# Performance work log

Measured on AMD Instinct MI355X. Metric: run time of the kernel, lower is better.

## Reference

```python
import jax, jax.numpy as jnp
import numpy as np
import math

H = 12  # num_heads
LOGIT_SCALE_MAX = math.log(1.0 / 0.01)  # ~4.60517


def setup_inputs() -> dict:
    key = jax.random.key(0)
    ks = jax.random.split(key, 4)
    L, N, C = 1024, 8, 768
    scale = (C // H) ** -0.5
    return {
        "x": jax.random.normal(ks[0], (L, N, C), jnp.float32),
        "in_proj_weight": jax.random.normal(ks[1], (3 * C, C), jnp.float32) * scale,
        "in_proj_bias": jnp.zeros((3 * C,), jnp.float32),
        "logit_scale": jnp.full((H, 1, 1), jnp.log(10.0), jnp.float32),
        "head_scale": jnp.ones((H, 1, 1), jnp.float32),
        "out_w": jax.random.normal(ks[2], (C, C), jnp.float32) * scale,
        "out_b": jnp.zeros((C,), jnp.float32),
    }


def _normalize(t, eps=1e-12):
    # torch F.normalize: x / max(||x||, eps)
    n = jnp.linalg.norm(t, axis=-1, keepdims=True)
    return t / jnp.maximum(n, eps)


def reference(x, in_proj_weight, in_proj_bias, logit_scale, head_scale, out_w, out_b):
    L, N, C = x.shape
    D = C // H
    qkv = x @ in_proj_weight.T + in_proj_bias  # (L, N, 3C)
    q, k, v = jnp.split(qkv, 3, axis=-1)

    def to_heads(t):  # (L, N, C) -> (N, H, L, D); matches view(L, N*H, D).transpose(0,1)
        return t.reshape(L, N, H, D).transpose(1, 2, 0, 3)

    q, k, v = to_heads(q), to_heads(k), to_heads(v)
    # scaled-cosine attention: cosine sim * clamped-exp learnable logit scale
    attn = jnp.einsum('nhld,nhmd->nhlm', _normalize(q), _normalize(k))  # (N,H,L,L)
    ls = jnp.exp(jnp.minimum(logit_scale, LOGIT_SCALE_MAX))  # (H,1,1)
    attn = attn * ls[None]
    attn = jax.nn.softmax(attn, axis=-1)
    o = jnp.einsum('nhlm,nhmd->nhld', attn, v)  # (N,H,L,D)
    o = o * head_scale[None]  # per-head scale
    o = o.transpose(2, 0, 1, 3).reshape(L, N, C)  # back to (L, N, C)
    return o @ out_w.T + out_b
```

## Files before the change

kernel.cpp:

```cpp
#include <hip/hip_runtime.h>
#include <stdint.h>
#include <math.h>

typedef unsigned short u16;
typedef _Float16 f16;
typedef __attribute__((ext_vector_type(4))) float f32x4;
typedef __attribute__((ext_vector_type(8))) f16 h8;
typedef __attribute__((ext_vector_type(4))) f16 h4;
typedef __attribute__((ext_vector_type(2))) f16 h2;
typedef __attribute__((ext_vector_type(2))) __fp16 fp16x2;
typedef __attribute__((ext_vector_type(4))) unsigned int u32x4;
typedef __attribute__((ext_vector_type(4))) unsigned short u16x4;
typedef __attribute__((ext_vector_type(8))) unsigned short u16x8;

typedef const __attribute__((address_space(1))) u16 gas_u16;
typedef __attribute__((address_space(3))) u16 las_u16;

#define MFMA32(a,b,c) __builtin_amdgcn_mfma_f32_16x16x32_f16((a),(b),(c),0,0,0)
#define MFMA16(a,b,c) __builtin_amdgcn_mfma_f32_16x16x16f16((a),(b),(c),0,0,0)

__device__ __forceinline__ float h2f(u16 h){ f16 x; __builtin_memcpy(&x,&h,2); return (float)x; }
__device__ __forceinline__ u16 f2h(float f){ f16 x = (f16)f; u16 u; __builtin_memcpy(&u,&x,2); return u; }

__device__ __forceinline__ float fast_exp2(float x){
#if __has_builtin(__builtin_amdgcn_exp2f)
  return __builtin_amdgcn_exp2f(x);
#else
  return exp2f(x);
#endif
}

__device__ __forceinline__ h2 pkrtz(float a, float b){
  fp16x2 t = __builtin_amdgcn_cvt_pkrtz(a, b);
  h2 r; __builtin_memcpy(&r, &t, 4);
  return r;
}

#define NA4 1572864
#define NB4 442368
#define NC4 147456
__global__ __launch_bounds__(256) void cvt3_kernel(
    const float* __restrict__ a, u16* __restrict__ da,
    const float* __restrict__ b, u16* __restrict__ db,
    const float* __restrict__ c, u16* __restrict__ dc)
{
  int i = blockIdx.x*256 + threadIdx.x;
  const float* s; u16* d; int off;
  if (i < NA4)            { s = a; d = da; off = i; }
  else if (i < NA4+NB4)   { s = b; d = db; off = i - NA4; }
  else if (i < NA4+NB4+NC4){ s = c; d = dc; off = i - NA4 - NB4; }
  else return;
  f32x4 v = ((const f32x4*)s)[off];
  u16x4 o;
  o[0]=f2h(v[0]); o[1]=f2h(v[1]); o[2]=f2h(v[2]); o[3]=f2h(v[3]);
  ((u16x4*)d)[off] = o;
}

__global__ __launch_bounds__(256) void gemm_kernel(
    const u16* __restrict__ A, const u16* __restrict__ B, const float* __restrict__ bias,
    int mode, u16* __restrict__ qh, u16* __restrict__ kh, u16* __restrict__ vh,
    float* __restrict__ outp, const float* __restrict__ lsb)
{
  __shared__ u16 lA[128*64];
  __shared__ u16 lB[128*64];
  const int tid = threadIdx.x;
  const int lane = tid & 63;
  const int w = tid >> 6, wr = w >> 1, wc = w & 1;
  const int lo = lane & 15, hi = lane >> 4;

  const int bx = blockIdx.x, by = blockIdx.y;

  f32x4 zero = {0.f,0.f,0.f,0.f};
  f32x4 acc[4][4];
#pragma unroll
  for (int a=0;a<4;a++)
#pragma unroll
    for (int b=0;b<4;b++) acc[a][b] = zero;
  const u16* Ag = A + (size_t)bx*128*768;
  const u16* Bg = B + (size_t)by*128*768;
  const int srow = tid >> 3;
  const int scol = (((tid & 7) ^ (srow & 7)) * 8);

  for (int kt = 0; kt < 768; kt += 64) {
#pragma unroll
    for (int j=0;j<4;j++) {
      __builtin_amdgcn_global_load_lds((gas_u16*)(Ag + (size_t)(j*32+srow)*768 + kt + scol), (las_u16*)(lA + j*2048 + tid*8), 16, 0, 0);
      __builtin_amdgcn_global_load_lds((gas_u16*)(Bg + (size_t)(j*32+srow)*768 + kt + scol), (las_u16*)(lB + j*2048 + tid*8), 16, 0, 0);
    }
    __syncthreads();
#pragma unroll
    for (int kk=0;kk<2;kk++) {
      h8 af[4], bfr[4];
#pragma unroll
      for (int mf=0; mf<4; mf++) {
        int r = wr*64 + mf*16 + lo;
        af[mf]  = *(const h8*)(lA + r*64 + (((hi + 4*kk) ^ (lo & 7)) * 8));
      }
#pragma unroll
      for (int nf=0; nf<4; nf++) {
        int r = wc*64 + nf*16 + lo;
        bfr[nf] = *(const h8*)(lB + r*64 + (((hi + 4*kk) ^ (lo & 7)) * 8));
      }
#pragma unroll
      for (int mf=0; mf<4; mf++)
#pragma unroll
        for (int nf=0; nf<4; nf++)
          acc[mf][nf] = MFMA32(af[mf], bfr[nf], acc[mf][nf]);
    }
    __syncthreads();
  }

  const int r0 = bx*128 + wr*64;
  const int j0 = by*128 + wc*64;
  if (mode == 0) {
    const int p = (j0 >= 1536) ? 2 : ((j0 >= 768) ? 1 : 0);
    const int c0 = j0 - p*768;
    const int hh = c0 >> 6;
    u16* dst = (p==0) ? qh : ((p==1) ? kh : vh);
    float bi[4];
#pragma unroll
    for (int nf=0;nf<4;nf++) bi[nf] = bias[j0 + nf*16 + lo];
    float qsc = 1.0f;
    if (p == 0) qsc = __expf(fminf(lsb[hh], 4.6051701859880913680f)) * 1.4426950408889634f;
    const bool dnorm = (p != 2);
#pragma unroll
    for (int mf=0; mf<4; mf++)
#pragma unroll
      for (int i=0;i<4;i++) {
        int r = r0 + mf*16 + 4*hi + i;
        int n = r & 7, l = r >> 3;
        float v[4]; float ss = 0.f;
#pragma unroll
        for (int nf=0;nf<4;nf++){ v[nf] = acc[mf][nf][i] + bi[nf]; ss += v[nf]*v[nf]; }
        float sc = 1.0f;
        if (dnorm) {
          ss += __shfl_xor(ss, 1);
          ss += __shfl_xor(ss, 2);
          ss += __shfl_xor(ss, 4);
          ss += __shfl_xor(ss, 8);
          sc = qsc / fmaxf(sqrtf(ss), 1e-12f);
        }
        size_t base = (((size_t)n*12 + hh)*1024 + l)*64;
#pragma unroll
        for (int nf=0;nf<4;nf++)
          dst[base + nf*16 + lo] = f2h(v[nf]*sc);
      }
  } else {
#pragma unroll
    for (int nf=0; nf<4; nf++) {
      int j = j0 + nf*16 + lo;
      float bi = bias[j];
#pragma unroll
      for (int mf=0; mf<4; mf++)
#pragma unroll
        for (int i=0;i<4;i++) {
          int r = r0 + mf*16 + 4*hi + i;
          outp[(size_t)r*768 + j] = acc[mf][nf][i] + bi;
        }
    }
  }
}

__global__ __launch_bounds__(256) void transpose_kernel(const u16* __restrict__ vh, u16* __restrict__ vt){
  __shared__ u16 tile[64*72];
  const int nh = blockIdx.y, lt = blockIdx.x, tid = threadIdx.x;
  const int r = tid >> 2, c0 = (tid & 3) * 16;
  const u16* src = vh + (size_t)nh*65536 + (size_t)(lt*64 + r)*64 + c0;
  u32x4 a = *(const u32x4*)src, b = *(const u32x4*)(src + 8);
  *(u32x4*)(tile + r*72 + c0)     = a;
  *(u32x4*)(tile + r*72 + c0 + 8) = b;
  __syncthreads();
  u16x8 o0, o1;
#pragma unroll
  for (int s=0;s<8;s++){ o0[s] = tile[(c0+s)*72 + r]; o1[s] = tile[(c0+8+s)*72 + r]; }
  u16* dst = vt + (size_t)nh*65536 + (size_t)r*1024 + lt*64 + c0;
  *(u16x8*)dst       = o0;
  *(u16x8*)(dst + 8) = o1;
}

__global__ __launch_bounds__(256) void flash_kernel(
    const u16* __restrict__ qh, const u16* __restrict__ kh, const u16* __restrict__ vt,
    u16* __restrict__ obuf, const float* __restrict__ hsv, const float* __restrict__ lsp)
{
  __shared__ u16 lK[2*64*72];
  __shared__ u16 lVT[2*64*72];
  const int lin = blockIdx.y*8 + blockIdx.x;
  const int xcd = lin & 7, g = lin >> 3;
  const int nh = xcd + 8*(g >> 3);
  const int qt = g & 7;
  const int h = nh % 12, n = nh / 12;
  const u16* Qp = qh + (size_t)nh*65536;
  const u16* Kp = kh + (size_t)nh*65536;
  const u16* Vp = vt + (size_t)nh*65536;
  const int tid = threadIdx.x, lane = tid & 63, w = tid >> 6;
  const int lo = lane & 15, hi = lane >> 4;

  h8 qa0, qa1, qb0, qb1;
  {
    const u16* qrow = Qp + (size_t)(qt*128 + w*32 + lo)*64 + hi*8;
    qa0 = *(const h8*)qrow;          qa1 = *(const h8*)(qrow + 32);
    qb0 = *(const h8*)(qrow + 1024); qb1 = *(const h8*)(qrow + 1024 + 32);
  }
  const f32x4 zero = {0.f,0.f,0.f,0.f};
  f32x4 oA[4] = {zero,zero,zero,zero};
  f32x4 oB[4] = {zero,zero,zero,zero};
  f32x4 lA4 = zero, lB4 = zero;
  const h4 ones = {(f16)1.f,(f16)1.f,(f16)1.f,(f16)1.f};

  float OFF;
  {
    float b = __expf(fminf(lsp[h], 4.6051701859880913680f)) * 1.4426950408889634f;
    OFF = fmaxf(b - 15.5f, 0.f);
  }

  const int sr = tid >> 2;
  const int sc = (tid & 3) * 16;
  u32x4 ka, kb, va, vb;
  ka = *(const u32x4*)(Kp + (size_t)sr*64 + sc);
  kb = *(const u32x4*)(Kp + (size_t)sr*64 + sc + 8);
  va = *(const u32x4*)(Vp + (size_t)sr*1024 + sc);
  vb = *(const u32x4*)(Vp + (size_t)sr*1024 + sc + 8);
  *(u32x4*)(lK  + sr*72 + sc)     = ka;
  *(u32x4*)(lK  + sr*72 + sc + 8) = kb;
  *(u32x4*)(lVT + sr*72 + sc)     = va;
  *(u32x4*)(lVT + sr*72 + sc + 8) = vb;
  __syncthreads();

  for (int t = 0; t < 16; ++t) {
    const u16* cK = lK  + (t&1)*4608;
    const u16* cV = lVT + (t&1)*4608;
    u16* nK = lK  + ((t&1)^1)*4608;
    u16* nV = lVT + ((t&1)^1)*4608;
    if (t < 15) {
      ka = *(const u32x4*)(Kp + (size_t)(t+1)*4096 + (size_t)sr*64 + sc);
      kb = *(const u32x4*)(Kp + (size_t)(t+1)*4096 + (size_t)sr*64 + sc + 8);
      va = *(const u32x4*)(Vp + (size_t)sr*1024 + (t+1)*64 + sc);
      vb = *(const u32x4*)(Vp + (size_t)sr*1024 + (t+1)*64 + sc + 8);
    }
    f32x4 sa[4], sb[4];
#pragma unroll
    for (int kf=0; kf<4; kf++) {
      const u16* krow = cK + (kf*16 + lo)*72 + hi*8;
      h8 k0 = *(const h8*)krow;
      h8 k1 = *(const h8*)(krow + 32);
      sa[kf] = MFMA32(k1, qa1, MFMA32(k0, qa0, zero));
      sb[kf] = MFMA32(k1, qb1, MFMA32(k0, qb0, zero));
    }
    if (OFF != 0.f) {
#pragma unroll
      for (int kf=0;kf<4;kf++)
#pragma unroll
        for (int i=0;i<4;i++) { sa[kf][i] -= OFF; sb[kf][i] -= OFF; }
    }
    h4 pa[4], pb[4];
#pragma unroll
    for (int kf=0;kf<4;kf++) {
      h2 a01 = pkrtz(fast_exp2(sa[kf][0]), fast_exp2(sa[kf][1]));
      h2 a23 = pkrtz(fast_exp2(sa[kf][2]), fast_exp2(sa[kf][3]));
      pa[kf] = __builtin_shufflevector(a01, a23, 0, 1, 2, 3);
      h2 b01 = pkrtz(fast_exp2(sb[kf][0]), fast_exp2(sb[kf][1]));
      h2 b23 = pkrtz(fast_exp2(sb[kf][2]), fast_exp2(sb[kf][3]));
      pb[kf] = __builtin_shufflevector(b01, b23, 0, 1, 2, 3);
    }
#pragma unroll
    for (int kf=0;kf<4;kf++) {
      lA4 = MFMA16(ones, pa[kf], lA4);
      lB4 = MFMA16(ones, pb[kf], lB4);
    }
#pragma unroll
    for (int db=0; db<4; db++) {
#pragma unroll
      for (int kf=0; kf<4; kf++) {
        h4 vf = *(const h4*)(cV + (db*16 + lo)*72 + kf*16 + hi*4);
        oA[db] = MFMA16(vf, pa[kf], oA[db]);
        oB[db] = MFMA16(vf, pb[kf], oB[db]);
      }
    }
    if (t < 15) {
      *(u32x4*)(nK + sr*72 + sc)     = ka;
      *(u32x4*)(nK + sr*72 + sc + 8) = kb;
      *(u32x4*)(nV + sr*72 + sc)     = va;
      *(u32x4*)(nV + sr*72 + sc + 8) = vb;
    }
    __syncthreads();
  }
  float hsc = hsv[h];
  float invA = hsc / lA4[0];
  float invB = hsc / lB4[0];
  int l0 = qt*128 + w*32 + lo;
  u16* dA = obuf + ((size_t)l0*8 + n)*768 + h*64;
  u16* dB = obuf + ((size_t)(l0+16)*8 + n)*768 + h*64;
#pragma unroll
  for (int db=0; db<4; db++) {
    u16x4 pk0, pk1;
#pragma unroll
    for (int i=0;i<4;i++) { pk0[i] = f2h(oA[db][i]*invA); pk1[i] = f2h(oB[db][i]*invB); }
    *(u16x4*)(dA + db*16 + hi*4) = pk0;
    *(u16x4*)(dB + db*16 + hi*4) = pk1;
  }
}

extern "C" void kernel_launch(void* const* d_in, const int* in_sizes, int n_in,
                              void* d_out, int out_size, void* d_ws, size_t ws_size,
                              hipStream_t stream)
{
  (void)in_sizes; (void)n_in; (void)out_size; (void)ws_size;
  const float* x  = (const float*)d_in[0];
  const float* w1 = (const float*)d_in[1];
  const float* b1 = (const float*)d_in[2];
  const float* ls = (const float*)d_in[3];
  const float* hs = (const float*)d_in[4];
  const float* w2 = (const float*)d_in[5];
  const float* b2 = (const float*)d_in[6];
  float* out = (float*)d_out;

  u16* x_bf  = (u16*)d_ws;
  u16* w1_bf = x_bf  + 6291456;
  u16* w2_bf = w1_bf + 1769472;
  u16* qh    = w2_bf + 589824;
  u16* kh    = qh    + 6291456;
  u16* vh    = kh    + 6291456;
  u16* vt    = vh    + 6291456;
  u16* ob    = x_bf;

  cvt3_kernel<<<8448, 256, 0, stream>>>(x, x_bf, w1, w1_bf, w2, w2_bf);
  gemm_kernel<<<dim3(64,18), 256, 0, stream>>>(x_bf, w1_bf, b1, 0, qh, kh, vh, nullptr, ls);
  transpose_kernel<<<dim3(16,96), 256, 0, stream>>>(vh, vt);
  flash_kernel<<<dim3(8,96), 256, 0, stream>>>(qh, kh, vt, ob, hs, ls);
  gemm_kernel<<<dim3(64,6), 256, 0, stream>>>(ob, w2_bf, b2, 1, nullptr, nullptr, nullptr, out, ls);
}
```

Measured before the change: 138.9 us.

## Double-buffer GEMM LDS tiles to overlap global loads with MFMA compute

```diff
diff --git a/kernel.cpp b/kernel.cpp
--- a/kernel.cpp
+++ b/kernel.cpp
@@ -61,8 +61,8 @@
     int mode, u16* __restrict__ qh, u16* __restrict__ kh, u16* __restrict__ vh,
     float* __restrict__ outp, const float* __restrict__ lsb)
 {
-  __shared__ u16 lA[128*64];
-  __shared__ u16 lB[128*64];
+  __shared__ u16 lA[2][128*64];
+  __shared__ u16 lB[2][128*64];
   const int tid = threadIdx.x;
   const int lane = tid & 63;
   const int w = tid >> 6, wr = w >> 1, wc = w & 1;
@@ -81,25 +81,38 @@
   const int srow = tid >> 3;
   const int scol = (((tid & 7) ^ (srow & 7)) * 8);
 
-  for (int kt = 0; kt < 768; kt += 64) {
-#pragma unroll
-    for (int j=0;j<4;j++) {
-      __builtin_amdgcn_global_load_lds((gas_u16*)(Ag + (size_t)(j*32+srow)*768 + kt + scol), (las_u16*)(lA + j*2048 + tid*8), 16, 0, 0);
-      __builtin_amdgcn_global_load_lds((gas_u16*)(Bg + (size_t)(j*32+srow)*768 + kt + scol), (las_u16*)(lB + j*2048 + tid*8), 16, 0, 0);
-    }
-    __syncthreads();
+#define STAGE(buf, kt) do { \
+    _Pragma("unroll") \
+    for (int j=0;j<4;j++) { \
+      __builtin_amdgcn_global_load_lds((gas_u16*)(Ag + (size_t)(j*32+srow)*768 + (kt) + scol), (las_u16*)(&lA[buf][j*2048 + tid*8]), 16, 0, 0); \
+      __builtin_amdgcn_global_load_lds((gas_u16*)(Bg + (size_t)(j*32+srow)*768 + (kt) + scol), (las_u16*)(&lB[buf][j*2048 + tid*8]), 16, 0, 0); \
+    } \
+  } while(0)
+
+  STAGE(0, 0);
+#pragma unroll
+  for (int t = 0; t < 12; ++t) {
+    const int cur = t & 1;
+    if (t < 11) {
+      STAGE(cur^1, (t+1)*64);
+      asm volatile("s_waitcnt vmcnt(8)" ::: "memory");
+    } else {
+      asm volatile("s_waitcnt vmcnt(0)" ::: "memory");
+    }
+    __builtin_amdgcn_sched_barrier(0);
+    __builtin_amdgcn_s_barrier();
 #pragma unroll
     for (int kk=0;kk<2;kk++) {
       h8 af[4], bfr[4];
 #pragma unroll
       for (int mf=0; mf<4; mf++) {
         int r = wr*64 + mf*16 + lo;
-        af[mf]  = *(const h8*)(lA + r*64 + (((hi + 4*kk) ^ (lo & 7)) * 8));
+        af[mf]  = *(const h8*)(&lA[cur][r*64 + (((hi + 4*kk) ^ (lo & 7)) * 8)]);
       }
 #pragma unroll
       for (int nf=0; nf<4; nf++) {
         int r = wc*64 + nf*16 + lo;
-        bfr[nf] = *(const h8*)(lB + r*64 + (((hi + 4*kk) ^ (lo & 7)) * 8));
+        bfr[nf] = *(const h8*)(&lB[cur][r*64 + (((hi + 4*kk) ^ (lo & 7)) * 8)]);
       }
 #pragma unroll
       for (int mf=0; mf<4; mf++)
@@ -107,8 +120,11 @@
         for (int nf=0; nf<4; nf++)
           acc[mf][nf] = MFMA32(af[mf], bfr[nf], acc[mf][nf]);
     }
-    __syncthreads();
-  }
+    asm volatile("s_waitcnt lgkmcnt(0)" ::: "memory");
+    __builtin_amdgcn_sched_barrier(0);
+    __builtin_amdgcn_s_barrier();
+  }
+#undef STAGE
 
   const int r0 = bx*128 + wr*64;
   const int j0 = by*128 + wc*64;
```

Result: faster. 130.6 us (-6.0%).
